# Kernel tuning notes

Measured on AMD Instinct MI355X. Metric: run time of the kernel, lower is better.

Reference implementation:

```python
import jax, jax.numpy as jnp
import numpy as np
import math

EPS_LN = 1e-5
TARGET_ACTIVITY = 0.1
THETA = 2.0 ** 16

B, NH, T, D, N = 2, 12, 2048, 768, 256


def layernorm(x):
    m = jnp.mean(x, axis=-1, keepdims=True)
    v = jnp.mean((x - m) ** 2, axis=-1, keepdims=True)
    return (x - m) / jnp.sqrt(v + EPS_LN)


def get_freqs(n):
    q = jnp.floor(jnp.arange(n, dtype=jnp.float32) / 2.0) * 2.0  # quantize by 2
    return 1.0 / (THETA ** (q / n)) / (2.0 * math.pi)


def rope(phases, v):
    ph = (phases % 1.0) * (2.0 * math.pi)
    c, s = jnp.cos(ph), jnp.sin(ph)
    even = v[..., 0::2]
    odd = v[..., 1::2]
    v_rot = jnp.stack((-odd, even), axis=-1).reshape(v.shape)  # interleaved rotate
    return v * c + v_rot * s


def setup_inputs() -> dict:
    key = jax.random.key(0)
    ks = jax.random.split(key, 5)
    std = 0.02
    return {
        "x": jax.random.normal(ks[0], (B, 1, T, D), dtype=jnp.float32),
        "encoder": jax.random.normal(ks[1], (NH, D, N), dtype=jnp.float32) * std,
        "encoder_v": jax.random.normal(ks[2], (NH, D, N), dtype=jnp.float32) * std,
        "decoder": jax.random.normal(ks[3], (NH * N, D), dtype=jnp.float32) * std,
        "scale": jnp.ones((D,), dtype=jnp.float32),
        "running_activity": jnp.ones((D,), dtype=jnp.float32) * TARGET_ACTIVITY,
    }


def reference(x, encoder, encoder_v, decoder, scale, running_activity):
    Bv, _, Tv, Dv = x.shape
    nh, _, Nv = encoder.shape

    # encode + ReLU sparsify: [B,1,T,D] @ [nh,D,N] -> [B,nh,T,N]
    x_latent = jnp.einsum('bztd,hdn->bhtn', x, encoder)
    x_sparse = jax.nn.relu(x_latent)

    # RoPE on Q=K=x_sparse
    freqs = get_freqs(Nv)  # [N]
    r_phases = jnp.arange(Tv, dtype=jnp.float32)[:, None] * freqs[None, :]  # [T,N]
    QR = rope(r_phases, x_sparse)
    KR = rope(r_phases, x_sparse)

    # non-softmax causal attention, strictly lower-triangular (diag=-1)
    scores = jnp.einsum('bhtn,bhsn->bhts', QR, KR)
    mask = jnp.tril(jnp.ones((Tv, Tv), dtype=scores.dtype), k=-1)
    scores = scores * mask
    yKV = jnp.einsum('bhts,bsd->bhtd', scores, x[:, 0])  # V = x

    yKV = layernorm(yKV)
    y_sparse = jax.nn.relu(jnp.einsum('bhtd,hdn->bhtn', yKV, encoder_v))
    xy_sparse = x_sparse * y_sparse  # [B,nh,T,N]; dropout=0 (eval)

    # [B,nh,T,N] -> [B,1,T,nh*N] @ [nh*N,D]
    flat = jnp.transpose(xy_sparse, (0, 2, 1, 3)).reshape(Bv, 1, Tv, nh * Nv)
    yMLP = flat @ decoder

    y = layernorm(yMLP)
    regulation = TARGET_ACTIVITY / (running_activity + 1e-6)
    y = y * jnp.sqrt(regulation) * scale

    return layernorm(x + y), xy_sparse
```

## Files before the change

kernel.cpp:

```cpp
#include <hip/hip_runtime.h>
#include <math.h>

#define TT 2048
#define DD 768
#define NN 256
#define NHH 12
#define BB 2
#define CH 512

typedef unsigned short u16;
typedef __attribute__((ext_vector_type(8))) short bf16x8;
typedef __attribute__((ext_vector_type(8))) unsigned short u16x8;
typedef __attribute__((ext_vector_type(4))) float f32x4;

static inline int imin(int a, int b) { return a < b ? a : b; }

__device__ __forceinline__ u16 f2b(float f) {
  union { float f; unsigned u; } a; a.f = f;
  unsigned r = a.u + 0x7FFF + ((a.u >> 16) & 1);
  return (u16)(r >> 16);
}
__device__ __forceinline__ float b2f(u16 h) {
  union { unsigned u; float f; } a; a.u = ((unsigned)h) << 16;
  return a.f;
}

__device__ __forceinline__ void async16(const void* g, void* l) {
  __builtin_amdgcn_global_load_lds(
      (const __attribute__((address_space(1))) unsigned*)g,
      (__attribute__((address_space(3))) unsigned*)l, 16, 0, 0);
}

__device__ __forceinline__ void stage128x32(
    const u16* __restrict__ gbase, size_t ld, u16* lds, int tid) {
  const int w = tid >> 6, l = tid & 63;
  const int r = l >> 2, kc = (l & 3) << 3;
#pragma unroll
  for (int q = 0; q < 2; ++q) {
    const int row0 = w * 32 + q * 16;
    async16(gbase + (size_t)(row0 + r) * ld + kc, lds + row0 * 32);
  }
}

__device__ __forceinline__ void stage64x32(
    const u16* __restrict__ gbase, size_t ld, u16* lds, int tid) {
  const int w = tid >> 6, l = tid & 63;
  const int r = w * 16 + (l >> 2), kc = (l & 3) << 3;
  async16(gbase + (size_t)r * ld + kc, lds + w * 512);
}

__device__ __forceinline__ void mfma_step(
    const u16* As, const u16* Bs, int wr, int wc, int lane, f32x4 acc[4][4]) {
  const int m16 = lane & 15, quad = lane >> 4;
  bf16x8 a[4], b[4];
#pragma unroll
  for (int i = 0; i < 4; ++i)
    a[i] = *(const bf16x8*)&As[(wr * 64 + i * 16 + m16) * 32 + quad * 8];
#pragma unroll
  for (int j = 0; j < 4; ++j)
    b[j] = *(const bf16x8*)&Bs[(wc * 64 + j * 16 + m16) * 32 + quad * 8];
#pragma unroll
  for (int i = 0; i < 4; ++i)
#pragma unroll
    for (int j = 0; j < 4; ++j)
      acc[i][j] = __builtin_amdgcn_mfma_f32_16x16x32_bf16(a[i], b[j], acc[i][j], 0, 0, 0);
}

__device__ __forceinline__ void copy_out128(
    const u16* buf, u16* g, size_t ld, int tid) {
#pragma unroll
  for (int s = 0; s < 8; ++s) {
    const int off = (s * 256 + tid) * 8;
    const int row = off >> 7, col = off & 127;
    *(u16x8*)&g[(size_t)row * ld + col] = *(const u16x8*)&buf[off];
  }
}

#define GEMM_PROLOGUE()                                            \
  __shared__ __attribute__((aligned(16))) u16 smem[32768];         \
  const int tid = threadIdx.x;                                     \
  const int w = tid >> 6, lane = tid & 63;                         \
  const int wr = w >> 1, wc = w & 1;                               \
  const int col16 = lane & 15, quad = lane >> 4;                   \
  f32x4 acc[4][4];                                                 \
  _Pragma("unroll") for (int i = 0; i < 4; ++i)                    \
  _Pragma("unroll") for (int j = 0; j < 4; ++j)                    \
      acc[i][j] = (f32x4){0.f, 0.f, 0.f, 0.f};

#define PIPELINED_K_LOOP64(ABASE, ALD, BBASE, BLD, KTOT)                    \
  {                                                                         \
    stage128x32((ABASE), (ALD), smem, tid);                                 \
    stage128x32((ABASE) + 32, (ALD), smem + 4096, tid);                     \
    stage128x32((BBASE), (BLD), smem + 8192, tid);                          \
    stage128x32((BBASE) + 32, (BLD), smem + 12288, tid);                    \
    const int np_ = (KTOT) / 64;                                            \
    for (int pp_ = 0; pp_ < np_; ++pp_) {                                   \
      u16* cb_ = (pp_ & 1) ? smem + 16384 : smem;                           \
      u16* nb_ = (pp_ & 1) ? smem : smem + 16384;                           \
      if (pp_ + 1 < np_) {                                                  \
        const int kn_ = (pp_ + 1) * 64;                                     \
        stage128x32((ABASE) + kn_, (ALD), nb_, tid);                        \
        stage128x32((ABASE) + kn_ + 32, (ALD), nb_ + 4096, tid);            \
        stage128x32((BBASE) + kn_, (BLD), nb_ + 8192, tid);                 \
        stage128x32((BBASE) + kn_ + 32, (BLD), nb_ + 12288, tid);           \
        asm volatile("s_waitcnt vmcnt(8)" ::: "memory");                    \
      } else {                                                              \
        asm volatile("s_waitcnt vmcnt(0)" ::: "memory");                    \
      }                                                                     \
      __builtin_amdgcn_s_barrier();                                         \
      __builtin_amdgcn_sched_barrier(0);                                    \
      mfma_step(cb_, cb_ + 8192, wr, wc, lane, acc);                        \
      mfma_step(cb_ + 4096, cb_ + 12288, wr, wc, lane, acc);                \
      __builtin_amdgcn_sched_barrier(0);                                    \
      __builtin_amdgcn_s_barrier();                                         \
    }                                                                       \
  }

__global__ __launch_bounds__(256) void cvt_bf16(
    const float* __restrict__ in, u16* __restrict__ out, size_t n4) {
  size_t i = ((size_t)blockIdx.x * 256 + threadIdx.x) * 4;
  if (i >= n4 * 4) return;
  float4 v = *(const float4*)&in[i];
  u16 o[4] = {f2b(v.x), f2b(v.y), f2b(v.z), f2b(v.w)};
  *(ushort4*)&out[i] = *(ushort4*)o;
}

__global__ __launch_bounds__(256) void tcvt_bf16(
    const float* __restrict__ in, u16* __restrict__ out, int R, int C,
    size_t inStride, size_t outStride) {
  __shared__ float tile[32][33];
  const float* ip = in + (size_t)blockIdx.z * inStride;
  u16* op = out + (size_t)blockIdx.z * outStride;
  const int c0 = blockIdx.x * 32, r0 = blockIdx.y * 32;
  const int tx = threadIdx.x & 31, ty = threadIdx.x >> 5;
#pragma unroll
  for (int p = 0; p < 4; ++p)
    tile[ty + p * 8][tx] = ip[(size_t)(r0 + ty + p * 8) * C + c0 + tx];
  __syncthreads();
#pragma unroll
  for (int p = 0; p < 4; ++p)
    op[(size_t)(c0 + ty + p * 8) * R + r0 + tx] = f2b(tile[tx][ty + p * 8]);
}

__global__ __launch_bounds__(256) void k_colsum(
    const u16* __restrict__ encvt, float* __restrict__ colsum) {
  const int row = blockIdx.x * 4 + (threadIdx.x >> 6);
  const int lane = threadIdx.x & 63;
  const u16* pr = encvt + (size_t)row * DD;
  float s = 0.f;
#pragma unroll
  for (int i = 0; i < 3; ++i) {
    ushort4 v = *(const ushort4*)&pr[(lane << 2) + i * 256];
    s += b2f(v.x) + b2f(v.y) + b2f(v.z) + b2f(v.w);
  }
#pragma unroll
  for (int off = 32; off; off >>= 1) s += __shfl_xor(s, off);
  if (lane == 0) colsum[row] = s;
}

__global__ __launch_bounds__(256) void k_cstab(float2* __restrict__ cs) {
  const int idx = blockIdx.x * 256 + threadIdx.x;
  const int t = idx >> 7, n2 = idx & 127;
  const float freq = exp2f((float)(2 * n2) * -0.0625f) * 0.15915494309189535f;
  const float phase = (float)t * freq;
  const float ph = (phase - floorf(phase)) * 6.283185307179586f;
  cs[idx] = make_float2(__cosf(ph), __sinf(ph));
}

__device__ __forceinline__ int swz8(int row) { return ((row >> 3) & 7) << 3; }

__global__ __launch_bounds__(256) void k1_encode(
    const u16* __restrict__ x16, const u16* __restrict__ enct,
    const float2* __restrict__ CS,
    u16* __restrict__ qr16, u16* __restrict__ qrt16) {
  const int h = blockIdx.z;
  const int m0 = blockIdx.x * 128, n0 = blockIdx.y * 128;
  GEMM_PROLOGUE();
  PIPELINED_K_LOOP64(x16 + (size_t)m0 * DD, DD,
                     enct + ((size_t)h * NN + n0) * DD, DD, DD);
  __syncthreads();
#pragma unroll
  for (int i = 0; i < 4; ++i)
#pragma unroll
    for (int j = 0; j < 4; ++j) {
      const int n = n0 + wc * 64 + j * 16 + col16;
      float rv[4], pv[4];
#pragma unroll
      for (int r = 0; r < 4; ++r) rv[r] = fmaxf(acc[i][j][r], 0.f);
#pragma unroll
      for (int r = 0; r < 4; ++r) pv[r] = __shfl_xor(rv[r], 1);
#pragma unroll
      for (int r = 0; r < 4; ++r) {
        const int lrow = wr * 64 + i * 16 + quad * 4 + r;
        const int t = (m0 + lrow) & (TT - 1);
        const float2 cs = CS[t * 128 + (n >> 1)];
        const float o = (n & 1) ? (rv[r] * cs.x + pv[r] * cs.y)
                                : (rv[r] * cs.x - pv[r] * cs.y);
        smem[lrow * 128 + ((wc * 64 + j * 16 + col16) ^ swz8(lrow))] = f2b(o);
      }
    }
  __syncthreads();
  const int bq = m0 >> 11, tb = m0 & (TT - 1);
  const size_t sl = (size_t)(bq * NHH + h);
  u16* qg = qr16 + (sl * TT + tb) * NN + n0;
#pragma unroll
  for (int s = 0; s < 8; ++s) {
    const int off = (s * 256 + tid) * 8;
    const int row = off >> 7, col = off & 127;
    *(u16x8*)&qg[(size_t)row * NN + col] =
        *(const u16x8*)&smem[row * 128 + (col ^ swz8(row))];
  }
#pragma unroll
  for (int s = 0; s < 8; ++s) {
    const int off = (s * 256 + tid) * 8;
    const int nr = off >> 7, tc = off & 127;
    const int sw = swz8(tc);
    u16 vals[8];
#pragma unroll
    for (int k = 0; k < 8; ++k) vals[k] = smem[(tc + k) * 128 + (nr ^ sw)];
    *(u16x8*)&qrt16[(sl * NN + n0 + nr) * TT + tb + tc] = *(u16x8*)vals;
  }
}

__global__ __launch_bounds__(256) void kS_band(
    const u16* __restrict__ qr16, u16* __restrict__ sb, int bh0) {
  const int z = blockIdx.y;
  const int bh = bh0 + z;
  const int cc = blockIdx.x / 10, rr = blockIdx.x % 10;
  int i = (int)((sqrtf(8.f * rr + 1.f) - 1.f) * 0.5f);
  while ((i + 1) * (i + 2) / 2 <= rr) ++i;
  while (i * (i + 1) / 2 > rr) --i;
  const int j = rr - i * (i + 1) / 2;
  const int t0 = (cc * 4 + i) * 128;
  const int s0 = cc * CH + j * 128;
  const u16* q = qr16 + (size_t)bh * TT * NN;
  GEMM_PROLOGUE();
  PIPELINED_K_LOOP64(q + (size_t)t0 * NN, NN, q + (size_t)s0 * NN, NN, NN);
  const bool diag = (i == j);
  __syncthreads();
#pragma unroll
  for (int ii = 0; ii < 4; ++ii)
#pragma unroll
    for (int jj = 0; jj < 4; ++jj) {
      const int s = s0 + wc * 64 + jj * 16 + col16;
#pragma unroll
      for (int r = 0; r < 4; ++r) {
        const int lrow = wr * 64 + ii * 16 + quad * 4 + r;
        const int t = t0 + lrow;
        float v = acc[ii][jj][r];
        if (diag && s >= t) v = 0.f;
        smem[lrow * 128 + wc * 64 + jj * 16 + col16] = f2b(v);
      }
    }
  __syncthreads();
  copy_out128(smem, sb + ((size_t)z * TT + t0) * CH + j * 128, CH, tid);
}

__global__ __launch_bounds__(256) void kB_all(
    const u16* __restrict__ xt16, const u16* __restrict__ qrt16,
    u16* __restrict__ h16, int bh0) {
  __shared__ __attribute__((aligned(16))) u16 sm[32768];
  u16* buf0 = sm;
  u16* buf1 = sm + 12288;
  u16* snap = sm + 24576;
  const int tid = threadIdx.x;
  const int w = tid >> 6, lane = tid & 63;
  const int m16 = lane & 15, quad = lane >> 4;
  const int z = blockIdx.z;
  const int bh = bh0 + z, b = bh / NHH;
  const int d0 = blockIdx.x * 64, n0 = blockIdx.y * 128;
  f32x4 acc[4][2];
#pragma unroll
  for (int i = 0; i < 4; ++i)
#pragma unroll
    for (int j = 0; j < 2; ++j) acc[i][j] = (f32x4){0.f, 0.f, 0.f, 0.f};
  const u16* Ab = xt16 + ((size_t)b * DD + d0) * TT;
  const u16* Bb = qrt16 + ((size_t)bh * NN + n0) * TT;
#define KB_STAGE(buf, k0)                                                   \
  {                                                                         \
    stage64x32(Ab + (k0), TT, (buf), tid);                                  \
    stage64x32(Ab + (k0) + 32, TT, (buf) + 2048, tid);                      \
    stage128x32(Bb + (k0), TT, (buf) + 4096, tid);                          \
    stage128x32(Bb + (k0) + 32, TT, (buf) + 8192, tid);                     \
  }
  for (int c = 0; c < 3; ++c) {
    const int kbase = c * CH;
    KB_STAGE(buf0, kbase);
    for (int s = 0; s < CH / 64; ++s) {
      u16* cb = (s & 1) ? buf1 : buf0;
      u16* nb = (s & 1) ? buf0 : buf1;
      if (s + 1 < CH / 64) {
        KB_STAGE(nb, kbase + (s + 1) * 64);
        asm volatile("s_waitcnt vmcnt(6)" ::: "memory");
      } else {
        asm volatile("s_waitcnt vmcnt(0)" ::: "memory");
      }
      __builtin_amdgcn_s_barrier();
      __builtin_amdgcn_sched_barrier(0);
#pragma unroll
      for (int half = 0; half < 2; ++half) {
        bf16x8 a[4], bb[2];
#pragma unroll
        for (int i = 0; i < 4; ++i)
          a[i] = *(const bf16x8*)&cb[half * 2048 + (i * 16 + m16) * 32 + quad * 8];
#pragma unroll
        for (int j = 0; j < 2; ++j)
          bb[j] = *(const bf16x8*)&cb[4096 + half * 4096 +
                                      (w * 32 + j * 16 + m16) * 32 + quad * 8];
#pragma unroll
        for (int i = 0; i < 4; ++i)
#pragma unroll
          for (int j = 0; j < 2; ++j)
            acc[i][j] = __builtin_amdgcn_mfma_f32_16x16x32_bf16(a[i], bb[j], acc[i][j], 0, 0, 0);
      }
      __builtin_amdgcn_sched_barrier(0);
      __builtin_amdgcn_s_barrier();
    }
#pragma unroll
    for (int i = 0; i < 4; ++i)
#pragma unroll
      for (int j = 0; j < 2; ++j)
#pragma unroll
        for (int r = 0; r < 4; ++r)
          snap[(i * 16 + quad * 4 + r) * 128 + w * 32 + j * 16 + m16] =
              f2b(acc[i][j][r]);
    __syncthreads();
    u16* hd = h16 + (size_t)(z * 3 + c) * DD * NN;
#pragma unroll
    for (int s4 = 0; s4 < 4; ++s4) {
      const int off = (s4 * 256 + tid) * 8;
      const int row = off >> 7, col = off & 127;
      *(u16x8*)&hd[(size_t)(d0 + row) * NN + n0 + col] = *(const u16x8*)&snap[off];
    }
    __syncthreads();
  }
#undef KB_STAGE
}

__device__ static const int TTORD[16] = {15, 11, 7, 14, 10, 6, 13, 9,
                                         5, 3, 12, 8, 4, 2, 1, 0};

__global__ __launch_bounds__(256) void kA_attn(
    const u16* __restrict__ qr16, const u16* __restrict__ h16,
    const u16* __restrict__ sb, const u16* __restrict__ xt16,
    u16* __restrict__ ykv16, int bh0) {
  __shared__ __attribute__((aligned(16))) u16 smem[32768];
  const int tid = threadIdx.x;
  const int w = tid >> 6, lane = tid & 63;
  const int wr = w >> 1, wc = w & 1;
  const int col16 = lane & 15, quad = lane >> 4;
  const int nwg = gridDim.x;
  const int bid = blockIdx.x;
  const int qq = nwg >> 3, r8 = nwg & 7;
  const int xcd = bid & 7, pos = bid >> 3;
  const int wg = (xcd < r8 ? xcd * (qq + 1) : r8 * (qq + 1) + (xcd - r8) * qq) + pos;
  const int z = wg / 96;
  const int tt = TTORD[(wg / 6) & 15];
  const int d0 = (wg % 6) * 128;
  const int bh = bh0 + z, b = bh / NHH;
  const int c = tt >> 2, it = tt & 3;
  const int t0 = tt * 128;
  f32x4 acc[4][4];
#pragma unroll
  for (int i = 0; i < 4; ++i)
#pragma unroll
    for (int j = 0; j < 4; ++j) acc[i][j] = (f32x4){0.f, 0.f, 0.f, 0.f};

  const int c4 = (c > 0) ? 4 : 0;
  const int nP = c4 + (it + 1) * 2;
  const u16* hs = h16 + ((size_t)(z * 3 + (c > 0 ? c - 1 : 0)) * DD + d0) * NN;
  const u16* qb = qr16 + ((size_t)bh * TT + t0) * NN;
  const u16* sbb = sb + ((size_t)z * TT + t0) * CH;
  const u16* xb = xt16 + ((size_t)b * DD + d0) * TT + c * CH;

#define KA_STAGE(buf, p)                                                  \
  {                                                                       \
    const u16 *pa_, *pb_; size_t la_, lb_;                                \
    if ((p) < c4) {                                                       \
      pa_ = qb + (p) * 64; la_ = NN;                                      \
      pb_ = hs + (p) * 64; lb_ = NN;                                      \
    } else {                                                              \
      const int q_ = (p) - c4;                                            \
      const int j_ = q_ >> 1, kk_ = (q_ & 1) << 6;                        \
      pa_ = sbb + j_ * 128 + kk_; la_ = CH;                               \
      pb_ = xb + j_ * 128 + kk_; lb_ = TT;                                \
    }                                                                     \
    stage128x32(pa_, la_, (buf), tid);                                    \
    stage128x32(pa_ + 32, la_, (buf) + 4096, tid);                        \
    stage128x32(pb_, lb_, (buf) + 8192, tid);                             \
    stage128x32(pb_ + 32, lb_, (buf) + 12288, tid);                       \
  }

  u16* bufA = smem;
  u16* bufB = smem + 16384;
  KA_STAGE(bufA, 0);
  for (int p = 0; p < nP; ++p) {
    u16* cb = (p & 1) ? bufB : bufA;
    u16* nb = (p & 1) ? bufA : bufB;
    if (p + 1 < nP) {
      KA_STAGE(nb, p + 1);
      asm volatile("s_waitcnt vmcnt(8)" ::: "memory");
    } else {
      asm volatile("s_waitcnt vmcnt(0)" ::: "memory");
    }
    __builtin_amdgcn_s_barrier();
    __builtin_amdgcn_sched_barrier(0);
    mfma_step(cb, cb + 8192, wr, wc, lane, acc);
    mfma_step(cb + 4096, cb + 12288, wr, wc, lane, acc);
    __builtin_amdgcn_sched_barrier(0);
    __builtin_amdgcn_s_barrier();
  }
#undef KA_STAGE

  __syncthreads();
#pragma unroll
  for (int i = 0; i < 4; ++i)
#pragma unroll
    for (int j = 0; j < 4; ++j)
#pragma unroll
      for (int r = 0; r < 4; ++r) {
        const int lrow = wr * 64 + i * 16 + quad * 4 + r;
        smem[lrow * 128 + wc * 64 + j * 16 + col16] = f2b(acc[i][j][r]);
      }
  __syncthreads();
  copy_out128(smem, ykv16 + ((size_t)z * TT + t0) * DD + d0, DD, tid);
}

__global__ __launch_bounds__(256) void k3_stats(
    const u16* __restrict__ ykv16, float* __restrict__ mu, float* __restrict__ rs) {
  const int row = blockIdx.x * 4 + (threadIdx.x >> 6);
  const int lane = threadIdx.x & 63;
  const u16* p = ykv16 + (size_t)row * DD;
  float sum = 0.f, sq = 0.f;
#pragma unroll
  for (int i = 0; i < 3; ++i) {
    ushort4 v = *(const ushort4*)&p[(lane << 2) + i * 256];
    float f0 = b2f(v.x), f1 = b2f(v.y), f2 = b2f(v.z), f3 = b2f(v.w);
    sum += f0 + f1 + f2 + f3;
    sq += f0 * f0 + f1 * f1 + f2 * f2 + f3 * f3;
  }
#pragma unroll
  for (int off = 32; off; off >>= 1) {
    sum += __shfl_xor(sum, off);
    sq += __shfl_xor(sq, off);
  }
  if (lane == 0) {
    float m = sum * (1.f / 768.f);
    float v = sq * (1.f / 768.f) - m * m;
    mu[row] = m;
    rs[row] = rsqrtf(v + 1e-5f);
  }
}

__global__ __launch_bounds__(256) void k4_xy(
    const u16* __restrict__ ykv16, const u16* __restrict__ encvt,
    const float2* __restrict__ CS,
    u16* __restrict__ qrxy, const float* __restrict__ mu,
    const float* __restrict__ rs, const float* __restrict__ colsum,
    float* __restrict__ out2, int bh0) {
  const int z = blockIdx.z;
  const int bh = bh0 + z, h = bh % NHH;
  const int t0 = blockIdx.x * 128, n0 = blockIdx.y * 128;
  GEMM_PROLOGUE();
  PIPELINED_K_LOOP64(ykv16 + ((size_t)z * TT + t0) * DD, DD,
                     encvt + ((size_t)h * NN + n0) * DD, DD, DD);
  __syncthreads();
#pragma unroll
  for (int i = 0; i < 4; ++i) {
    float muv[4], rsv[4];
#pragma unroll
    for (int r = 0; r < 4; ++r) {
      const int lrow = z * TT + t0 + wr * 64 + i * 16 + quad * 4 + r;
      muv[r] = mu[lrow];
      rsv[r] = rs[lrow];
    }
#pragma unroll
    for (int j = 0; j < 4; ++j) {
      const int n = n0 + wc * 64 + j * 16 + col16;
      const float csum = colsum[h * NN + n];
#pragma unroll
      for (int r = 0; r < 4; ++r) {
        const int lrow = wr * 64 + i * 16 + quad * 4 + r;
        const int t = t0 + lrow;
        const float ys = fmaxf(rsv[r] * acc[i][j][r] - rsv[r] * muv[r] * csum, 0.f);
        const size_t gi = ((size_t)bh * TT + t) * NN + n;
        const unsigned pq = *(const unsigned*)&qrxy[gi & ~(size_t)1];
        const float lo = b2f((u16)pq), hi = b2f((u16)(pq >> 16));
        const float2 cs = CS[t * 128 + (n >> 1)];
        const float xs = (n & 1) ? (hi * cs.x - lo * cs.y)
                                 : (lo * cs.x + hi * cs.y);
        const float val = ys * xs;
        out2[gi] = val;
        smem[lrow * 128 + wc * 64 + j * 16 + col16] = f2b(val);
      }
    }
  }
  __syncthreads();
  copy_out128(smem, qrxy + ((size_t)bh * TT + t0) * NN + n0, NN, tid);
}

__global__ __launch_bounds__(256) void k5_mlp(
    const u16* __restrict__ xyq, const u16* __restrict__ dect,
    float* __restrict__ ymlp) {
  __shared__ __attribute__((aligned(16))) u16 sm[24576];
  const int tid = threadIdx.x;
  const int w = tid >> 6, lane = tid & 63;
  const int wr = w >> 1, wc = w & 1;
  const int m16 = lane & 15, quad = lane >> 4;
  const int m0 = blockIdx.x * 64, d0 = blockIdx.y * 64;
  f32x4 acc[2][2];
#pragma unroll
  for (int i = 0; i < 2; ++i)
#pragma unroll
    for (int j = 0; j < 2; ++j) acc[i][j] = (f32x4){0.f, 0.f, 0.f, 0.f};
  const int ar = w * 16 + (lane >> 2);
  const int m = m0 + ar;
  const int b = m >> 11, t = m & (TT - 1);
  const int kc = (lane & 3) << 3;
#define K5_STAGE(buf, k0)                                                   \
  {                                                                         \
    const int hh_ = (k0) >> 8;                                              \
    const int kk_ = ((k0) & 255) + kc;                                      \
    const u16* ap_ = xyq + ((size_t)(b * NHH + hh_) * TT + t) * NN;         \
    async16(ap_ + kk_, (buf) + w * 512);                                    \
    async16(ap_ + kk_ + 32, (buf) + 2048 + w * 512);                        \
    stage64x32(dect + (size_t)d0 * (NHH * NN) + (k0), NHH * NN,             \
               (buf) + 4096, tid);                                          \
    stage64x32(dect + (size_t)d0 * (NHH * NN) + (k0) + 32, NHH * NN,        \
               (buf) + 6144, tid);                                          \
  }
  const int NK = (NHH * NN) / 64;
  u16 *b0 = sm, *b1 = sm + 8192, *b2 = sm + 16384;
  K5_STAGE(b0, 0);
  K5_STAGE(b1, 64);
  for (int s = 0; s < NK; ++s) {
    if (s + 2 < NK) {
      K5_STAGE(b2, (s + 2) * 64);
      asm volatile("s_waitcnt vmcnt(8)" ::: "memory");
    } else if (s + 1 < NK) {
      asm volatile("s_waitcnt vmcnt(4)" ::: "memory");
    } else {
      asm volatile("s_waitcnt vmcnt(0)" ::: "memory");
    }
    __builtin_amdgcn_s_barrier();
    __builtin_amdgcn_sched_barrier(0);
#pragma unroll
    for (int half = 0; half < 2; ++half) {
      bf16x8 a[2], bb[2];
#pragma unroll
      for (int i = 0; i < 2; ++i)
        a[i] = *(const bf16x8*)&b0[half * 2048 + (wr * 32 + i * 16 + m16) * 32 + quad * 8];
#pragma unroll
      for (int j = 0; j < 2; ++j)
        bb[j] = *(const bf16x8*)&b0[4096 + half * 2048 + (wc * 32 + j * 16 + m16) * 32 + quad * 8];
#pragma unroll
      for (int i = 0; i < 2; ++i)
#pragma unroll
        for (int j = 0; j < 2; ++j)
          acc[i][j] = __builtin_amdgcn_mfma_f32_16x16x32_bf16(a[i], bb[j], acc[i][j], 0, 0, 0);
    }
    __builtin_amdgcn_sched_barrier(0);
    __builtin_amdgcn_s_barrier();
    u16* tmp = b0; b0 = b1; b1 = b2; b2 = tmp;
  }
#undef K5_STAGE
#pragma unroll
  for (int i = 0; i < 2; ++i)
#pragma unroll
    for (int j = 0; j < 2; ++j) {
      const int d = d0 + wc * 32 + j * 16 + m16;
#pragma unroll
      for (int r = 0; r < 4; ++r) {
        const int mm = m0 + wr * 32 + i * 16 + quad * 4 + r;
        ymlp[(size_t)mm * DD + d] = acc[i][j][r];
      }
    }
}

__global__ __launch_bounds__(256) void k6_final(
    const float* __restrict__ ymlp, const float* __restrict__ x,
    const float* __restrict__ scale, const float* __restrict__ ra,
    float* __restrict__ out1) {
  const int row = blockIdx.x;
  const int tid = threadIdx.x;
  const int wid = tid >> 6, lane = tid & 63;
  __shared__ float red[8];
  float v[3];
  float sum = 0.f, sq = 0.f;
#pragma unroll
  for (int j = 0; j < 3; ++j) {
    v[j] = ymlp[(size_t)row * DD + tid + j * 256];
    sum += v[j]; sq += v[j] * v[j];
  }
#pragma unroll
  for (int off = 32; off; off >>= 1) { sum += __shfl_xor(sum, off); sq += __shfl_xor(sq, off); }
  if (lane == 0) { red[wid] = sum; red[4 + wid] = sq; }
  __syncthreads();
  sum = red[0] + red[1] + red[2] + red[3];
  sq = red[4] + red[5] + red[6] + red[7];
  const float m1 = sum * (1.f / 768.f);
  const float r1 = rsqrtf(sq * (1.f / 768.f) - m1 * m1 + 1e-5f);
  float z[3];
  float sum2 = 0.f, sq2 = 0.f;
#pragma unroll
  for (int j = 0; j < 3; ++j) {
    const int d = tid + j * 256;
    float y = (v[j] - m1) * r1 * sqrtf(0.1f / (ra[d] + 1e-6f)) * scale[d];
    z[j] = x[(size_t)row * DD + d] + y;
    sum2 += z[j]; sq2 += z[j] * z[j];
  }
  __syncthreads();
#pragma unroll
  for (int off = 32; off; off >>= 1) { sum2 += __shfl_xor(sum2, off); sq2 += __shfl_xor(sq2, off); }
  if (lane == 0) { red[wid] = sum2; red[4 + wid] = sq2; }
  __syncthreads();
  sum2 = red[0] + red[1] + red[2] + red[3];
  sq2 = red[4] + red[5] + red[6] + red[7];
  const float m2 = sum2 * (1.f / 768.f);
  const float r2 = rsqrtf(sq2 * (1.f / 768.f) - m2 * m2 + 1e-5f);
#pragma unroll
  for (int j = 0; j < 3; ++j)
    out1[(size_t)row * DD + tid + j * 256] = (z[j] - m2) * r2;
}

extern "C" void kernel_launch(void* const* d_in, const int* in_sizes, int n_in,
                              void* d_out, int out_size, void* d_ws, size_t ws_size,
                              hipStream_t stream) {
  const float* x = (const float*)d_in[0];
  const float* enc = (const float*)d_in[1];
  const float* encv = (const float*)d_in[2];
  const float* dec = (const float*)d_in[3];
  const float* scale = (const float*)d_in[4];
  const float* ra = (const float*)d_in[5];
  float* out1 = (float*)d_out;
  float* out2 = out1 + (size_t)BB * TT * DD;
  float* ymlp = out1;

  const int NS = BB * NHH;
  unsigned char* p = (unsigned char*)d_ws;
  u16* X16 = (u16*)p;    p += (size_t)BB * TT * DD * 2;
  u16* XT16 = (u16*)p;   p += (size_t)BB * DD * TT * 2;
  u16* ENCT = (u16*)p;   p += (size_t)NHH * NN * DD * 2;
  u16* ENCVT = (u16*)p;  p += (size_t)NHH * NN * DD * 2;
  u16* DECT = (u16*)p;   p += (size_t)DD * NHH * NN * 2;
  u16* QR16 = (u16*)p;   p += (size_t)NS * TT * NN * 2;
  u16* QRT16 = (u16*)p;  p += (size_t)NS * NN * TT * 2;
  float* COLSUM = (float*)p; p += (size_t)NHH * NN * 4;
  float2* CS = (float2*)p;   p += (size_t)TT * (NN / 2) * sizeof(float2);
  const size_t SLICE_B = (size_t)TT * CH * 2 + 3 * (size_t)DD * NN * 2 +
                         (size_t)TT * DD * 2 + (size_t)TT * 8;
  size_t fixed = (size_t)(p - (unsigned char*)d_ws);
  size_t rem = (ws_size > fixed) ? ws_size - fixed : 0;
  int GSmax = (int)(rem / SLICE_B);
  if (GSmax < 1) GSmax = 1;
  if (GSmax > NS) GSmax = NS;
  const int ngrp = (NS + GSmax - 1) / GSmax;
  const int GS = (NS + ngrp - 1) / ngrp;
  u16* SB = (u16*)p;     p += (size_t)GS * TT * CH * 2;
  u16* H16 = (u16*)p;    p += (size_t)GS * 3 * DD * NN * 2;
  u16* YKV16 = (u16*)p;  p += (size_t)GS * TT * DD * 2;
  float* MU = (float*)p; p += (size_t)GS * TT * 4;
  float* RS = (float*)p; p += (size_t)GS * TT * 4;

  cvt_bf16<<<dim3((BB * TT * DD) / 1024), 256, 0, stream>>>(x, X16, (size_t)BB * TT * DD / 4);
  tcvt_bf16<<<dim3(DD / 32, TT / 32, BB), 256, 0, stream>>>(
      x, XT16, TT, DD, (size_t)TT * DD, (size_t)DD * TT);
  tcvt_bf16<<<dim3(NN / 32, DD / 32, NHH), 256, 0, stream>>>(
      enc, ENCT, DD, NN, (size_t)DD * NN, (size_t)NN * DD);
  tcvt_bf16<<<dim3(NN / 32, DD / 32, NHH), 256, 0, stream>>>(
      encv, ENCVT, DD, NN, (size_t)DD * NN, (size_t)NN * DD);
  tcvt_bf16<<<dim3(DD / 32, (NHH * NN) / 32, 1), 256, 0, stream>>>(
      dec, DECT, NHH * NN, DD, 0, 0);
  k_colsum<<<dim3(NHH * NN / 4), 256, 0, stream>>>(ENCVT, COLSUM);
  k_cstab<<<dim3(TT * (NN / 2) / 256), 256, 0, stream>>>(CS);

  k1_encode<<<dim3(BB * TT / 128, NN / 128, NHH), 256, 0, stream>>>(
      X16, ENCT, CS, QR16, QRT16);

  for (int bh0 = 0; bh0 < NS; bh0 += GS) {
    const int gs = imin(GS, NS - bh0);
    kS_band<<<dim3(40, gs), 256, 0, stream>>>(QR16, SB, bh0);
    kB_all<<<dim3(DD / 64, NN / 128, gs), 256, 0, stream>>>(
        XT16, QRT16, H16, bh0);
    kA_attn<<<dim3(96 * gs), 256, 0, stream>>>(
        QR16, H16, SB, XT16, YKV16, bh0);
    k3_stats<<<dim3(gs * TT / 4), 256, 0, stream>>>(YKV16, MU, RS);
    k4_xy<<<dim3(TT / 128, NN / 128, gs), 256, 0, stream>>>(
        YKV16, ENCVT, CS, QR16, MU, RS, COLSUM, out2, bh0);
  }

  k5_mlp<<<dim3(BB * TT / 64, DD / 64), 256, 0, stream>>>(QR16, DECT, ymlp);
  k6_final<<<dim3(BB * TT), 256, 0, stream>>>(ymlp, x, scale, ra, out1);
}
```

Before: 379.9 us.

## Swizzle LDS tiles, fuse layernorm stats into attention epilogue, stage QR in LDS

Applies an XOR swizzle to the K-chunk column of every LDS-staged 32-wide tile, on both the async stores and the MFMA fragment reads, to cut LDS bank conflicts. Removes the separate stats kernel: the attention epilogue reduces per-row sums and sums of squares across lanes and atomically adds them into global buffers, which are zeroed by a memset each group. The xy epilogue now async-loads the QR tile into shared memory instead of reading it scattered from global. The atomics add contention and order-dependent rounding, and the memset adds a launch per group.

```diff
diff --git a/kernel.cpp b/kernel.cpp
--- a/kernel.cpp
+++ b/kernel.cpp
@@ -31,22 +31,25 @@
       (__attribute__((address_space(3))) unsigned*)l, 16, 0, 0);
 }
 
+#define KSWZ(row) (((row) >> 1) & 3)
+
 __device__ __forceinline__ void stage128x32(
     const u16* __restrict__ gbase, size_t ld, u16* lds, int tid) {
   const int w = tid >> 6, l = tid & 63;
-  const int r = l >> 2, kc = (l & 3) << 3;
 #pragma unroll
   for (int q = 0; q < 2; ++q) {
-    const int row0 = w * 32 + q * 16;
-    async16(gbase + (size_t)(row0 + r) * ld + kc, lds + row0 * 32);
+    const int row = w * 32 + q * 16 + (l >> 2);
+    const int kc = ((l & 3) ^ KSWZ(row)) << 3;
+    async16(gbase + (size_t)row * ld + kc, lds + (w * 32 + q * 16) * 32);
   }
 }
 
 __device__ __forceinline__ void stage64x32(
     const u16* __restrict__ gbase, size_t ld, u16* lds, int tid) {
   const int w = tid >> 6, l = tid & 63;
-  const int r = w * 16 + (l >> 2), kc = (l & 3) << 3;
-  async16(gbase + (size_t)r * ld + kc, lds + w * 512);
+  const int row = w * 16 + (l >> 2);
+  const int kc = ((l & 3) ^ KSWZ(row)) << 3;
+  async16(gbase + (size_t)row * ld + kc, lds + w * 512);
 }
 
 __device__ __forceinline__ void mfma_step(
@@ -54,11 +57,15 @@
   const int m16 = lane & 15, quad = lane >> 4;
   bf16x8 a[4], b[4];
 #pragma unroll
-  for (int i = 0; i < 4; ++i)
-    a[i] = *(const bf16x8*)&As[(wr * 64 + i * 16 + m16) * 32 + quad * 8];
-#pragma unroll
-  for (int j = 0; j < 4; ++j)
-    b[j] = *(const bf16x8*)&Bs[(wc * 64 + j * 16 + m16) * 32 + quad * 8];
+  for (int i = 0; i < 4; ++i) {
+    const int row = wr * 64 + i * 16 + m16;
+    a[i] = *(const bf16x8*)&As[row * 32 + ((quad ^ KSWZ(row)) << 3)];
+  }
+#pragma unroll
+  for (int j = 0; j < 4; ++j) {
+    const int row = wc * 64 + j * 16 + m16;
+    b[j] = *(const bf16x8*)&Bs[row * 32 + ((quad ^ KSWZ(row)) << 3)];
+  }
 #pragma unroll
   for (int i = 0; i < 4; ++i)
 #pragma unroll
@@ -301,12 +308,17 @@
       for (int half = 0; half < 2; ++half) {
         bf16x8 a[4], bb[2];
 #pragma unroll
-        for (int i = 0; i < 4; ++i)
-          a[i] = *(const bf16x8*)&cb[half * 2048 + (i * 16 + m16) * 32 + quad * 8];
-#pragma unroll
-        for (int j = 0; j < 2; ++j)
-          bb[j] = *(const bf16x8*)&cb[4096 + half * 4096 +
-                                      (w * 32 + j * 16 + m16) * 32 + quad * 8];
+        for (int i = 0; i < 4; ++i) {
+          const int row = i * 16 + m16;
+          a[i] = *(const bf16x8*)&cb[half * 2048 + row * 32 +
+                                     ((quad ^ KSWZ(row)) << 3)];
+        }
+#pragma unroll
+        for (int j = 0; j < 2; ++j) {
+          const int row = w * 32 + j * 16 + m16;
+          bb[j] = *(const bf16x8*)&cb[4096 + half * 4096 + row * 32 +
+                                      ((quad ^ KSWZ(row)) << 3)];
+        }
 #pragma unroll
         for (int i = 0; i < 4; ++i)
 #pragma unroll
@@ -343,7 +355,8 @@
 __global__ __launch_bounds__(256) void kA_attn(
     const u16* __restrict__ qr16, const u16* __restrict__ h16,
     const u16* __restrict__ sb, const u16* __restrict__ xt16,
-    u16* __restrict__ ykv16, int bh0) {
+    u16* __restrict__ ykv16, float* __restrict__ SUMB,
+    float* __restrict__ SQB, int bh0) {
   __shared__ __attribute__((aligned(16))) u16 smem[32768];
   const int tid = threadIdx.x;
   const int w = tid >> 6, lane = tid & 63;
@@ -351,9 +364,9 @@
   const int col16 = lane & 15, quad = lane >> 4;
   const int nwg = gridDim.x;
   const int bid = blockIdx.x;
-  const int qq = nwg >> 3, r8 = nwg & 7;
+  const int qn = nwg >> 3, r8 = nwg & 7;
   const int xcd = bid & 7, pos = bid >> 3;
-  const int wg = (xcd < r8 ? xcd * (qq + 1) : r8 * (qq + 1) + (xcd - r8) * qq) + pos;
+  const int wg = (xcd < r8 ? xcd * (qn + 1) : r8 * (qn + 1) + (xcd - r8) * qn) + pos;
   const int z = wg / 96;
   const int tt = TTORD[(wg / 6) & 15];
   const int d0 = (wg % 6) * 128;
@@ -413,6 +426,11 @@
 #undef KA_STAGE
 
   __syncthreads();
+  float fsum[4][4], fsq[4][4];
+#pragma unroll
+  for (int i = 0; i < 4; ++i)
+#pragma unroll
+    for (int r = 0; r < 4; ++r) { fsum[i][r] = 0.f; fsq[i][r] = 0.f; }
 #pragma unroll
   for (int i = 0; i < 4; ++i)
 #pragma unroll
@@ -420,43 +438,37 @@
 #pragma unroll
       for (int r = 0; r < 4; ++r) {
         const int lrow = wr * 64 + i * 16 + quad * 4 + r;
-        smem[lrow * 128 + wc * 64 + j * 16 + col16] = f2b(acc[i][j][r]);
-      }
+        const u16 hv = f2b(acc[i][j][r]);
+        smem[lrow * 128 + wc * 64 + j * 16 + col16] = hv;
+        const float vr = b2f(hv);
+        fsum[i][r] += vr;
+        fsq[i][r] += vr * vr;
+      }
+#pragma unroll
+  for (int i = 0; i < 4; ++i)
+#pragma unroll
+    for (int r = 0; r < 4; ++r) {
+      float s = fsum[i][r], q2 = fsq[i][r];
+#pragma unroll
+      for (int off = 1; off < 16; off <<= 1) {
+        s += __shfl_xor(s, off);
+        q2 += __shfl_xor(q2, off);
+      }
+      if (col16 == 0) {
+        const int grow = z * TT + t0 + wr * 64 + i * 16 + quad * 4 + r;
+        atomicAdd(&SUMB[grow], s);
+        atomicAdd(&SQB[grow], q2);
+      }
+    }
   __syncthreads();
   copy_out128(smem, ykv16 + ((size_t)z * TT + t0) * DD + d0, DD, tid);
-}
-
-__global__ __launch_bounds__(256) void k3_stats(
-    const u16* __restrict__ ykv16, float* __restrict__ mu, float* __restrict__ rs) {
-  const int row = blockIdx.x * 4 + (threadIdx.x >> 6);
-  const int lane = threadIdx.x & 63;
-  const u16* p = ykv16 + (size_t)row * DD;
-  float sum = 0.f, sq = 0.f;
-#pragma unroll
-  for (int i = 0; i < 3; ++i) {
-    ushort4 v = *(const ushort4*)&p[(lane << 2) + i * 256];
-    float f0 = b2f(v.x), f1 = b2f(v.y), f2 = b2f(v.z), f3 = b2f(v.w);
-    sum += f0 + f1 + f2 + f3;
-    sq += f0 * f0 + f1 * f1 + f2 * f2 + f3 * f3;
-  }
-#pragma unroll
-  for (int off = 32; off; off >>= 1) {
-    sum += __shfl_xor(sum, off);
-    sq += __shfl_xor(sq, off);
-  }
-  if (lane == 0) {
-    float m = sum * (1.f / 768.f);
-    float v = sq * (1.f / 768.f) - m * m;
-    mu[row] = m;
-    rs[row] = rsqrtf(v + 1e-5f);
-  }
 }
 
 __global__ __launch_bounds__(256) void k4_xy(
     const u16* __restrict__ ykv16, const u16* __restrict__ encvt,
     const float2* __restrict__ CS,
-    u16* __restrict__ qrxy, const float* __restrict__ mu,
-    const float* __restrict__ rs, const float* __restrict__ colsum,
+    u16* __restrict__ qrxy, const float* __restrict__ SUMB,
+    const float* __restrict__ SQB, const float* __restrict__ colsum,
     float* __restrict__ out2, int bh0) {
   const int z = blockIdx.z;
   const int bh = bh0 + z, h = bh % NHH;
@@ -464,34 +476,47 @@
   GEMM_PROLOGUE();
   PIPELINED_K_LOOP64(ykv16 + ((size_t)z * TT + t0) * DD, DD,
                      encvt + ((size_t)h * NN + n0) * DD, DD, DD);
+  {
+    const u16* qg = qrxy + ((size_t)bh * TT + t0) * NN + n0;
+#pragma unroll
+    for (int s = 0; s < 8; ++s) {
+      const int row = s * 16 + w * 4 + (lane >> 4);
+      const int col = (lane & 15) * 8;
+      async16(qg + (size_t)row * NN + col,
+              smem + 16384 + (s * 256 + w * 64) * 8);
+    }
+  }
+  asm volatile("s_waitcnt vmcnt(0)" ::: "memory");
   __syncthreads();
 #pragma unroll
   for (int i = 0; i < 4; ++i) {
     float muv[4], rsv[4];
 #pragma unroll
     for (int r = 0; r < 4; ++r) {
-      const int lrow = z * TT + t0 + wr * 64 + i * 16 + quad * 4 + r;
-      muv[r] = mu[lrow];
-      rsv[r] = rs[lrow];
+      const int grow = z * TT + t0 + wr * 64 + i * 16 + quad * 4 + r;
+      const float m_ = SUMB[grow] * (1.f / 768.f);
+      muv[r] = m_;
+      rsv[r] = rsqrtf(SQB[grow] * (1.f / 768.f) - m_ * m_ + 1e-5f);
     }
 #pragma unroll
     for (int j = 0; j < 4; ++j) {
-      const int n = n0 + wc * 64 + j * 16 + col16;
+      const int lcol = wc * 64 + j * 16 + col16;
+      const int n = n0 + lcol;
       const float csum = colsum[h * NN + n];
 #pragma unroll
       for (int r = 0; r < 4; ++r) {
         const int lrow = wr * 64 + i * 16 + quad * 4 + r;
         const int t = t0 + lrow;
         const float ys = fmaxf(rsv[r] * acc[i][j][r] - rsv[r] * muv[r] * csum, 0.f);
-        const size_t gi = ((size_t)bh * TT + t) * NN + n;
-        const unsigned pq = *(const unsigned*)&qrxy[gi & ~(size_t)1];
+        const unsigned pq =
+            *(const unsigned*)&smem[16384 + lrow * 128 + (lcol & ~1)];
         const float lo = b2f((u16)pq), hi = b2f((u16)(pq >> 16));
         const float2 cs = CS[t * 128 + (n >> 1)];
         const float xs = (n & 1) ? (hi * cs.x - lo * cs.y)
                                  : (lo * cs.x + hi * cs.y);
         const float val = ys * xs;
-        out2[gi] = val;
-        smem[lrow * 128 + wc * 64 + j * 16 + col16] = f2b(val);
+        out2[((size_t)bh * TT + t) * NN + n] = val;
+        smem[lrow * 128 + lcol] = f2b(val);
       }
     }
   }
@@ -516,7 +541,7 @@
   const int ar = w * 16 + (lane >> 2);
   const int m = m0 + ar;
   const int b = m >> 11, t = m & (TT - 1);
-  const int kc = (lane & 3) << 3;
+  const int kc = (((lane & 3) ^ KSWZ(ar)) << 3);
 #define K5_STAGE(buf, k0)                                                   \
   {                                                                         \
     const int hh_ = (k0) >> 8;                                              \
@@ -548,11 +573,17 @@
     for (int half = 0; half < 2; ++half) {
       bf16x8 a[2], bb[2];
 #pragma unroll
-      for (int i = 0; i < 2; ++i)
-        a[i] = *(const bf16x8*)&b0[half * 2048 + (wr * 32 + i * 16 + m16) * 32 + quad * 8];
-#pragma unroll
-      for (int j = 0; j < 2; ++j)
-        bb[j] = *(const bf16x8*)&b0[4096 + half * 2048 + (wc * 32 + j * 16 + m16) * 32 + quad * 8];
+      for (int i = 0; i < 2; ++i) {
+        const int row = wr * 32 + i * 16 + m16;
+        a[i] = *(const bf16x8*)&b0[half * 2048 + row * 32 +
+                                   ((quad ^ KSWZ(row)) << 3)];
+      }
+#pragma unroll
+      for (int j = 0; j < 2; ++j) {
+        const int row = wc * 32 + j * 16 + m16;
+        bb[j] = *(const bf16x8*)&b0[4096 + half * 2048 + row * 32 +
+                                    ((quad ^ KSWZ(row)) << 3)];
+      }
 #pragma unroll
       for (int i = 0; i < 2; ++i)
 #pragma unroll
@@ -659,8 +690,8 @@
   u16* SB = (u16*)p;     p += (size_t)GS * TT * CH * 2;
   u16* H16 = (u16*)p;    p += (size_t)GS * 3 * DD * NN * 2;
   u16* YKV16 = (u16*)p;  p += (size_t)GS * TT * DD * 2;
-  float* MU = (float*)p; p += (size_t)GS * TT * 4;
-  float* RS = (float*)p; p += (size_t)GS * TT * 4;
+  float* SUMB = (float*)p; p += (size_t)GS * TT * 4;
+  float* SQB = (float*)p;  p += (size_t)GS * TT * 4;
 
   cvt_bf16<<<dim3((BB * TT * DD) / 1024), 256, 0, stream>>>(x, X16, (size_t)BB * TT * DD / 4);
   tcvt_bf16<<<dim3(DD / 32, TT / 32, BB), 256, 0, stream>>>(
@@ -679,14 +710,14 @@
 
   for (int bh0 = 0; bh0 < NS; bh0 += GS) {
     const int gs = imin(GS, NS - bh0);
+    hipMemsetAsync(SUMB, 0, (size_t)GS * TT * 8, stream);
     kS_band<<<dim3(40, gs), 256, 0, stream>>>(QR16, SB, bh0);
     kB_all<<<dim3(DD / 64, NN / 128, gs), 256, 0, stream>>>(
         XT16, QRT16, H16, bh0);
     kA_attn<<<dim3(96 * gs), 256, 0, stream>>>(
-        QR16, H16, SB, XT16, YKV16, bh0);
-    k3_stats<<<dim3(gs * TT / 4), 256, 0, stream>>>(YKV16, MU, RS);
+        QR16, H16, SB, XT16, YKV16, SUMB, SQB, bh0);
     k4_xy<<<dim3(TT / 128, NN / 128, gs), 256, 0, stream>>>(
-        YKV16, ENCVT, CS, QR16, MU, RS, COLSUM, out2, bh0);
+        YKV16, ENCVT, CS, QR16, SUMB, SQB, COLSUM, out2, bh0);
   }
 
   k5_mlp<<<dim3(BB * TT / 64, DD / 64), 256, 0, stream>>>(QR16, DECT, ymlp);
```

Result: no change. 381.4 us (+0.4%).
